# Optimization experiments

Measured on AMD Instinct MI355X. Metric: run time of the kernel, lower is better.

## Reference

```python
import jax, jax.numpy as jnp
import numpy as np
from jax import lax

B, N, D = 8, 1024, 512
HEAD_DIM = 64          # = num_attention_heads arg (used as split chunk size in torch)
H = D // HEAD_DIM      # actual number of heads = 8
TOPK = 32
EPS = 1e-5


def setup_inputs() -> dict:
    key = jax.random.key(0)
    ks = jax.random.split(key, 20)
    s = 0.02
    inp = {
        "src": jax.random.normal(ks[0], (B, N, D), jnp.float32),
        "tgt": jax.random.normal(ks[1], (B, N, D), jnp.float32),
        "Wq": jax.random.normal(ks[2], (D, D), jnp.float32) * s,
        "bq": jnp.zeros((D,), jnp.float32),
        "Wk": jax.random.normal(ks[3], (D, D), jnp.float32) * s,
        "bk": jnp.zeros((D,), jnp.float32),
        "Wv": jax.random.normal(ks[4], (D, D), jnp.float32) * s,
        "bv": jnp.zeros((D,), jnp.float32),
        "W1": jax.random.normal(ks[5], (D, D), jnp.float32) * s,
        "b1": jnp.zeros((D,), jnp.float32),
        "W2": jax.random.normal(ks[6], (D, D), jnp.float32) * s,
        "b2": jnp.zeros((D,), jnp.float32),
        "g1": jnp.ones((D,), jnp.float32),
        "be1": jnp.zeros((D,), jnp.float32),
        "g2": jnp.ones((D,), jnp.float32),
        "be2": jnp.zeros((D,), jnp.float32),
    }
    return inp


def _layer_norm(x, g, b):
    mu = jnp.mean(x, axis=-1, keepdims=True)
    var = jnp.mean(jnp.square(x - mu), axis=-1, keepdims=True)
    return (x - mu) * lax.rsqrt(var + EPS) * g + b


def _to_heads(x):
    # torch: cat(split(x, HEAD_DIM, dim=-1), dim=0) -> head-major leading dim
    # [B, N, D] -> [H*B, N, HEAD_DIM]
    return x.reshape(B, N, H, HEAD_DIM).transpose(2, 0, 1, 3).reshape(H * B, N, HEAD_DIM)


def reference(src, tgt, Wq, bq, Wk, bk, Wv, bv, W1, b1, W2, b2, g1, be1, g2, be2):
    q = _to_heads(tgt @ Wq + bq) / jnp.sqrt(jnp.float32(D))  # scale by hidden_dim**0.5 (as in source)
    k = _to_heads(src @ Wk + bk)
    v = _to_heads(src @ Wv + bv)

    scores = jnp.einsum('hqd,hkd->hqk', q, k)  # [H*B, N, N]

    idx = lax.top_k(scores, TOPK)[1]                       # [H*B, N, TOPK]
    vals = jnp.take_along_axis(scores, idx, axis=-1)       # gather top-k values
    sparse = jnp.full_like(scores, -jnp.inf)
    hb = jnp.arange(H * B)[:, None, None]
    qn = jnp.arange(N)[None, :, None]
    sparse = sparse.at[hb, qn, idx].set(vals)

    attn = jax.nn.softmax(sparse, axis=-1)                 # rows have TOPK finite entries
    out = jnp.einsum('hqk,hkd->hqd', attn, v)              # [H*B, N, HEAD_DIM]
    # torch: cat(split(out, B, dim=0), dim=-1) -> [B, N, D]
    out = out.reshape(H, B, N, HEAD_DIM).transpose(1, 2, 0, 3).reshape(B, N, D)

    x = _layer_norm(tgt + out, g1, be1)
    ff = jax.nn.relu(x @ W1 + b1) @ W2 + b2   # dropout = identity in eval mode
    return _layer_norm(x + ff, g2, be2)
```

## Files before the change

kernel.cpp:

```cpp
#include <hip/hip_runtime.h>
#include <math.h>

#define NSQ 1024
#define DM  512
#define HDIM 64
#define TOPK 32
#define QSTR 72
#define PCAP 64

typedef unsigned short u16;
typedef __attribute__((ext_vector_type(8))) short bf16x8;
typedef __attribute__((ext_vector_type(4))) float f32x4;

#define MFMA_B16(A,B,C) __builtin_amdgcn_mfma_f32_16x16x32_bf16(A,B,C,0,0,0)

__device__ __forceinline__ unsigned f2b(float x) {
    unsigned u = __float_as_uint(x);
    return (u + 0x7FFFu + ((u >> 16) & 1u)) >> 16;
}
__device__ __forceinline__ float b2f(unsigned h) { return __uint_as_float(h << 16); }
__device__ __forceinline__ unsigned ordu(float f) {
    unsigned b = __float_as_uint(f);
    return b ^ (0x80000000u | (unsigned)((int)b >> 31));
}
__device__ __forceinline__ float iordu(unsigned u) {
    unsigned b = (u & 0x80000000u) ? (u ^ 0x80000000u) : ~u;
    return __uint_as_float(b);
}

__global__ __launch_bounds__(256) void conv2(
    const float* __restrict__ tgt, const float* __restrict__ src,
    u16* __restrict__ Thi, u16* __restrict__ Tlo,
    u16* __restrict__ Shi, u16* __restrict__ Slo)
{
    const int z = blockIdx.y;
    const float* x = z ? src : tgt;
    u16* hi = z ? Shi : Thi;
    u16* lo = z ? Slo : Tlo;
    int idx = blockIdx.x * 256 + threadIdx.x;
    float4 v = ((const float4*)x)[idx];
    float f[4] = {v.x, v.y, v.z, v.w};
    ushort4 hv, lv;
    unsigned h;
    h = f2b(f[0]); hv.x = (u16)h; lv.x = (u16)f2b(f[0] - b2f(h));
    h = f2b(f[1]); hv.y = (u16)h; lv.y = (u16)f2b(f[1] - b2f(h));
    h = f2b(f[2]); hv.z = (u16)h; lv.z = (u16)f2b(f[2] - b2f(h));
    h = f2b(f[3]); hv.w = (u16)h; lv.w = (u16)f2b(f[3] - b2f(h));
    ((ushort4*)hi)[idx] = hv;
    ((ushort4*)lo)[idx] = lv;
}

__global__ __launch_bounds__(256) void wconv5(
    const float* __restrict__ Wq, const float* __restrict__ Wk,
    const float* __restrict__ Wv, const float* __restrict__ W1,
    const float* __restrict__ W2, u16* __restrict__ planes)
{
    __shared__ float T[32][33];
    const int wsel = blockIdx.z;
    const float* W = (wsel == 0) ? Wq : (wsel == 1) ? Wk : (wsel == 2) ? Wv
                   : (wsel == 3) ? W1 : W2;
    u16* thi = planes + (size_t)wsel * 2 * DM * DM;
    u16* tlo = thi + (size_t)DM * DM;
    const int tx = threadIdx.x & 31, ty = threadIdx.x >> 5;
    const int n0 = blockIdx.x * 32, k0 = blockIdx.y * 32;
#pragma unroll
    for (int p = 0; p < 4; ++p) {
        int r = ty + p * 8;
        T[r][tx] = W[(size_t)(k0 + r) * DM + n0 + tx];
    }
    __syncthreads();
#pragma unroll
    for (int p = 0; p < 4; ++p) {
        int rr = ty + p * 8;
        float val = T[tx][rr];
        unsigned h = f2b(val);
        size_t off = (size_t)(n0 + rr) * DM + k0 + tx;
        thi[off] = (u16)h;
        tlo[off] = (u16)f2b(val - b2f(h));
    }
}

template<int SPLIT, int RELU, int OUTMODE>
__global__ __launch_bounds__(256) void mm512(
    const u16* __restrict__ Ah_g, const u16* __restrict__ Al_g,
    const u16* __restrict__ Bh_g, const u16* __restrict__ Bl_g,
    const float* __restrict__ bias, const float* __restrict__ R,
    float scale, float* __restrict__ outF,
    u16* __restrict__ outHi, u16* __restrict__ outLo)
{
    __shared__ u16 Ah[128 * 40], Bh[128 * 40];
    __shared__ u16 Al[SPLIT ? 128 * 40 : 8], Bl[SPLIT ? 128 * 40 : 8];
    const int tid = threadIdx.x, lane = tid & 63, w = tid >> 6;
    const int wr = (w >> 1) * 64, wc = (w & 1) * 64;
    const int ml = lane & 15, q8 = (lane >> 4) * 8, q4 = (lane >> 4) * 4;
    const int row0 = blockIdx.x * 128, col0 = blockIdx.y * 128;
    const int sm = tid >> 2, sk = (tid & 3) * 8;

    f32x4 acc[4][4];
#pragma unroll
    for (int i = 0; i < 4; ++i)
#pragma unroll
        for (int j = 0; j < 4; ++j) acc[i][j] = {0.f, 0.f, 0.f, 0.f};

    for (int k0 = 0; k0 < DM; k0 += 32) {
#pragma unroll
        for (int p = 0; p < 2; ++p) {
            int m = sm + p * 64;
            *(uint4*)&Ah[m * 40 + sk] = *(const uint4*)&Ah_g[(size_t)(row0 + m) * DM + k0 + sk];
            *(uint4*)&Bh[m * 40 + sk] = *(const uint4*)&Bh_g[(size_t)(col0 + m) * DM + k0 + sk];
            if (SPLIT) {
                *(uint4*)&Al[m * 40 + sk] = *(const uint4*)&Al_g[(size_t)(row0 + m) * DM + k0 + sk];
                *(uint4*)&Bl[m * 40 + sk] = *(const uint4*)&Bl_g[(size_t)(col0 + m) * DM + k0 + sk];
            }
        }
        __syncthreads();
        bf16x8 a_h[4], b_h[4], a_l[4], b_l[4];
#pragma unroll
        for (int i = 0; i < 4; ++i) {
            a_h[i] = *(const bf16x8*)&Ah[(wr + i * 16 + ml) * 40 + q8];
            b_h[i] = *(const bf16x8*)&Bh[(wc + i * 16 + ml) * 40 + q8];
            if (SPLIT) {
                a_l[i] = *(const bf16x8*)&Al[(wr + i * 16 + ml) * 40 + q8];
                b_l[i] = *(const bf16x8*)&Bl[(wc + i * 16 + ml) * 40 + q8];
            }
        }
#pragma unroll
        for (int i = 0; i < 4; ++i)
#pragma unroll
            for (int j = 0; j < 4; ++j) {
                acc[i][j] = MFMA_B16(a_h[i], b_h[j], acc[i][j]);
                if (SPLIT) {
                    acc[i][j] = MFMA_B16(a_h[i], b_l[j], acc[i][j]);
                    acc[i][j] = MFMA_B16(a_l[i], b_h[j], acc[i][j]);
                    acc[i][j] = MFMA_B16(a_l[i], b_l[j], acc[i][j]);
                }
            }
        __syncthreads();
    }

    float bcol[4];
#pragma unroll
    for (int j = 0; j < 4; ++j) bcol[j] = bias[col0 + wc + j * 16 + ml];
#pragma unroll
    for (int i = 0; i < 4; ++i)
#pragma unroll
        for (int j = 0; j < 4; ++j)
#pragma unroll
            for (int r = 0; r < 4; ++r) {
                int gm = row0 + wr + i * 16 + q4 + r;
                int gn = col0 + wc + j * 16 + ml;
                float t = acc[i][j][r] + bcol[j];
                if (RELU) t = fmaxf(t, 0.f);
                t *= scale;
                size_t off = (size_t)gm * DM + gn;
                if (OUTMODE == 0) {
                    if (R) t += R[off];
                    outF[off] = t;
                } else if (OUTMODE == 1) {
                    unsigned hb2 = f2b(t);
                    outHi[off] = (u16)hb2;
                    outLo[off] = (u16)f2b(t - b2f(hb2));
                } else {
                    outHi[off] = (u16)f2b(t);
                }
            }
}

__global__ __launch_bounds__(256, 4) void attn_fused(
    const u16* __restrict__ qhi, const u16* __restrict__ qlo,
    const u16* __restrict__ khi, const u16* __restrict__ klo,
    const u16* __restrict__ vhi, u16* __restrict__ ao)
{
    __shared__ u16 Qh[16 * QSTR], Ql[16 * QSTR];
    __shared__ float statS[4][16], statQ[4][16];
    __shared__ int   cntW[4][16];
    __shared__ float pval[16][PCAP];
    __shared__ int   pcol[16][PCAP];
    __shared__ unsigned loU[16];

    const int tid = threadIdx.x, lane = tid & 63, w = tid >> 6;
    const int ml = lane & 15, quad = lane >> 4, q8 = quad * 8;
    const int hb = blockIdx.y, h = hb >> 3, b = hb & 7;
    const int r0 = blockIdx.x * 16;

    {
        int t2 = tid & 127, m = t2 >> 3, k8 = (t2 & 7) * 8;
        const u16* sp = (tid < 128) ? qhi : qlo;
        u16* dst = (tid < 128) ? Qh : Ql;
        *(uint4*)&dst[m * QSTR + k8] =
            *(const uint4*)&sp[((size_t)(b * NSQ + r0 + m)) * DM + h * HDIM + k8];
    }
    __syncthreads();

    bf16x8 a_h0 = *(const bf16x8*)&Qh[ml * QSTR + q8];
    bf16x8 a_h1 = *(const bf16x8*)&Qh[ml * QSTR + 32 + q8];
    bf16x8 a_l0 = *(const bf16x8*)&Ql[ml * QSTR + q8];
    bf16x8 a_l1 = *(const bf16x8*)&Ql[ml * QSTR + 32 + q8];

    const u16* khp = khi + ((size_t)(b * NSQ + w * 256 + ml)) * DM + h * HDIM + q8;
    const u16* klp = klo + ((size_t)(b * NSQ + w * 256 + ml)) * DM + h * HDIM + q8;

    f32x4 acc[16];
#pragma unroll
    for (int t = 0; t < 16; ++t) {
        bf16x8 bh0 = *(const bf16x8*)(khp);
        bf16x8 bh1 = *(const bf16x8*)(khp + 32);
        bf16x8 bl0 = *(const bf16x8*)(klp);
        bf16x8 bl1 = *(const bf16x8*)(klp + 32);
        f32x4 a0 = {0.f, 0.f, 0.f, 0.f}, a1 = {0.f, 0.f, 0.f, 0.f};
        a0 = MFMA_B16(a_h0, bh0, a0);
        a0 = MFMA_B16(a_h1, bh1, a0);
        a0 = MFMA_B16(a_l0, bh0, a0);
        a0 = MFMA_B16(a_l1, bh1, a0);
        a1 = MFMA_B16(a_h0, bl0, a1);
        a1 = MFMA_B16(a_h1, bl1, a1);
        a1 = MFMA_B16(a_l0, bl0, a1);
        a1 = MFMA_B16(a_l1, bl1, a1);
        acc[t] = a0 + a1;
        khp += 16 * DM;
        klp += 16 * DM;
    }

    float s1[4] = {0.f, 0.f, 0.f, 0.f}, s2[4] = {0.f, 0.f, 0.f, 0.f};
#pragma unroll
    for (int t = 0; t < 16; ++t)
#pragma unroll
        for (int r = 0; r < 4; ++r) {
            float v = acc[t][r];
            s1[r] += v;
            s2[r] = fmaf(v, v, s2[r]);
        }
#pragma unroll
    for (int off = 8; off; off >>= 1)
#pragma unroll
        for (int r = 0; r < 4; ++r) {
            s1[r] += __shfl_xor(s1[r], off);
            s2[r] += __shfl_xor(s2[r], off);
        }
    if (ml == 0)
#pragma unroll
        for (int r = 0; r < 4; ++r) {
            statS[w][quad * 4 + r] = s1[r];
            statQ[w][quad * 4 + r] = s2[r];
        }
    __syncthreads();

    float mu[4], sg[4], lo_f[4], hi_f[4];
    unsigned lo_u[4], hi_u[4];
    int clo[4];
#pragma unroll
    for (int r = 0; r < 4; ++r) {
        int row = quad * 4 + r;
        float S = statS[0][row] + statS[1][row] + statS[2][row] + statS[3][row];
        float Q = statQ[0][row] + statQ[1][row] + statQ[2][row] + statQ[3][row];
        mu[r] = S * (1.f / 1024.f);
        sg[r] = sqrtf(fmaxf(Q * (1.f / 1024.f) - mu[r] * mu[r], 0.f)) + 1e-20f;
        lo_f[r] = mu[r] - 8.f * sg[r];
        hi_f[r] = mu[r] + 8.f * sg[r];
        lo_u[r] = ordu(lo_f[r]);
        hi_u[r] = ordu(hi_f[r]);
        clo[r] = 1024;
    }

    int done = 0;
    for (int iter = 0; iter < 24; ++iter) {
        float mid_f[4]; unsigned mid_u[4];
#pragma unroll
        for (int r = 0; r < 4; ++r) {
            if (!((done >> r) & 1)) {
                float fr; unsigned um;
                if (iter == 0)      fr = mu[r] + 1.70f * sg[r];
                else if (iter == 1) fr = mu[r] + ((clo[r] == 1024) ? 1.38f : 2.15f) * sg[r];
                else {
                    um = lo_u[r] + ((hi_u[r] - lo_u[r]) >> 1);
                    fr = iordu(um); mid_u[r] = um; mid_f[r] = fr;
                    continue;
                }
                um = ordu(fr);
                if (um <= lo_u[r] || um >= hi_u[r]) {
                    um = lo_u[r] + ((hi_u[r] - lo_u[r]) >> 1);
                    fr = iordu(um);
                }
                mid_u[r] = um; mid_f[r] = fr;
            } else { mid_u[r] = lo_u[r]; mid_f[r] = lo_f[r]; }
        }
        int c[4] = {0, 0, 0, 0};
#pragma unroll
        for (int t = 0; t < 16; ++t)
#pragma unroll
            for (int r = 0; r < 4; ++r) c[r] += (acc[t][r] > mid_f[r]) ? 1 : 0;
#pragma unroll
        for (int off = 8; off; off >>= 1)
#pragma unroll
            for (int r = 0; r < 4; ++r) c[r] += __shfl_xor(c[r], off);
        if (ml == 0)
#pragma unroll
            for (int r = 0; r < 4; ++r) cntW[w][quad * 4 + r] = c[r];
        __syncthreads();
        int tot[4];
#pragma unroll
        for (int r = 0; r < 4; ++r) {
            int row = quad * 4 + r;
            tot[r] = cntW[0][row] + cntW[1][row] + cntW[2][row] + cntW[3][row];
        }
        __syncthreads();
#pragma unroll
        for (int r = 0; r < 4; ++r) {
            if (!((done >> r) & 1)) {
                if (tot[r] >= TOPK) {
                    lo_u[r] = mid_u[r]; lo_f[r] = mid_f[r]; clo[r] = tot[r];
                    if (tot[r] <= PCAP) done |= 1 << r;
                } else {
                    hi_u[r] = mid_u[r]; hi_f[r] = mid_f[r];
                }
                if (hi_u[r] - lo_u[r] <= 1u) done |= 1 << r;
            }
        }
        if (__all(done == 15)) break;
    }

    {
        int c[4] = {0, 0, 0, 0};
#pragma unroll
        for (int t = 0; t < 16; ++t)
#pragma unroll
            for (int r = 0; r < 4; ++r) c[r] += (acc[t][r] > lo_f[r]) ? 1 : 0;
#pragma unroll
        for (int off = 8; off; off >>= 1)
#pragma unroll
            for (int r = 0; r < 4; ++r) c[r] += __shfl_xor(c[r], off);
        if (ml == 0)
#pragma unroll
            for (int r = 0; r < 4; ++r) cntW[w][quad * 4 + r] = c[r];
        if (w == 0 && ml == 0)
#pragma unroll
            for (int r = 0; r < 4; ++r) loU[quad * 4 + r] = lo_u[r];
    }
    __syncthreads();

    int base[4];
#pragma unroll
    for (int r = 0; r < 4; ++r) {
        int row = quad * 4 + r, s = 0;
#pragma unroll
        for (int ww = 0; ww < 4; ++ww) s += (ww < w) ? cntW[ww][row] : 0;
        base[r] = s;
    }

    const unsigned lmask = (1u << ml) - 1u;
#pragma unroll
    for (int t = 0; t < 16; ++t)
#pragma unroll
        for (int r = 0; r < 4; ++r) {
            bool sel = acc[t][r] > lo_f[r];
            unsigned long long bm = __ballot(sel);
            unsigned mq = (unsigned)(bm >> (quad * 16)) & 0xFFFFu;
            if (sel) {
                int slot = base[r] + __popc(mq & lmask);
                if (slot < PCAP) {
                    pval[quad * 4 + r][slot] = acc[t][r];
                    pcol[quad * 4 + r][slot] = w * 256 + t * 16 + ml;
                }
            }
            base[r] += __popc(mq);
        }
    __syncthreads();

    const u16* vb = vhi + ((size_t)b * NSQ) * DM + h * HDIM + lane;
    for (int rr = 0; rr < 4; ++rr) {
        const int row = w * 4 + rr;
        int n = cntW[0][row] + cntW[1][row] + cntW[2][row] + cntW[3][row];
        if (n > PCAP) n = PCAP;
        float val = (lane < n) ? pval[row][lane] : 0.f;
        int   col = (lane < n) ? pcol[row][lane] : 0;
        unsigned uv = (lane < n) ? ordu(val) : 0u;

        unsigned blo = loU[row], bhi = 0xFFFFFFFFu;
        while (bhi - blo > 1u) {
            unsigned mid = blo + ((bhi - blo) >> 1);
            int c = __popcll(__ballot(uv > mid));
            if (c >= TOPK) { blo = mid; if (c == TOPK) break; }
            else bhi = mid;
        }
        bool sel = uv > blo;
        int excess = __popcll(__ballot(sel)) - TOPK;
        while (excess > 0) {
            int mycol = (sel && uv == blo + 1u) ? col : -1;
            int cmx = mycol;
#pragma unroll
            for (int off = 32; off; off >>= 1) cmx = max(cmx, __shfl_xor(cmx, off));
            if (sel && mycol >= 0 && col == cmx) sel = false;
            excess--;
        }

        float vsel = sel ? val : -INFINITY;
        float m = vsel;
#pragma unroll
        for (int off = 32; off; off >>= 1) m = fmaxf(m, __shfl_xor(m, off));
        float e = sel ? __expf(val - m) : 0.f;
        float s = e;
#pragma unroll
        for (int off = 32; off; off >>= 1) s += __shfl_xor(s, off);
        float p = e * (1.f / s);

        unsigned long long bm = __ballot(sel);
        int slot = __popcll(bm & ((1ull << lane) - 1ull));
        if (sel) { pval[row][slot] = p; pcol[row][slot] = col; }

        float accv = 0.f;
#pragma unroll
        for (int t0 = 0; t0 < TOPK; t0 += 8) {
            float pp[8]; int cc[8]; u16 vv[8];
#pragma unroll
            for (int j = 0; j < 8; ++j) { pp[j] = pval[row][t0 + j]; cc[j] = pcol[row][t0 + j]; }
#pragma unroll
            for (int j = 0; j < 8; ++j) vv[j] = vb[(size_t)cc[j] * DM];
#pragma unroll
            for (int j = 0; j < 8; ++j) accv = fmaf(pp[j], b2f(vv[j]), accv);
        }
        ao[((size_t)(b * NSQ + r0 + row)) * DM + h * HDIM + lane] = (u16)f2b(accv);
    }
}

__global__ __launch_bounds__(256) void ln_fused(
    const float* __restrict__ a, const u16* __restrict__ addb,
    const float* __restrict__ g, const float* __restrict__ be,
    float* __restrict__ outF, u16* __restrict__ outHi)
{
    __shared__ float red[4][2];
    const int row = blockIdx.x, tid = threadIdx.x, w = tid >> 6;
    float2 v = ((const float2*)(a + (size_t)row * DM))[tid];
    if (addb) {
        ushort2 ab = ((const ushort2*)(addb + (size_t)row * DM))[tid];
        v.x += b2f(ab.x); v.y += b2f(ab.y);
    }
    float s = v.x + v.y, q = v.x * v.x + v.y * v.y;
#pragma unroll
    for (int o = 32; o; o >>= 1) { s += __shfl_xor(s, o); q += __shfl_xor(q, o); }
    if ((tid & 63) == 0) { red[w][0] = s; red[w][1] = q; }
    __syncthreads();
    float S = red[0][0] + red[1][0] + red[2][0] + red[3][0];
    float Q = red[0][1] + red[1][1] + red[2][1] + red[3][1];
    float mu = S * (1.f / DM);
    float var = Q * (1.f / DM) - mu * mu;
    float rs = rsqrtf(var + 1e-5f);
    float2 gv = ((const float2*)g)[tid];
    float2 bv = ((const float2*)be)[tid];
    float2 o;
    o.x = (v.x - mu) * rs * gv.x + bv.x;
    o.y = (v.y - mu) * rs * gv.y + bv.y;
    if (outF) ((float2*)(outF + (size_t)row * DM))[tid] = o;
    if (outHi) {
        ushort2 hv; hv.x = (u16)f2b(o.x); hv.y = (u16)f2b(o.y);
        ((ushort2*)(outHi + (size_t)row * DM))[tid] = hv;
    }
}

extern "C" void kernel_launch(void* const* d_in, const int* in_sizes, int n_in,
                              void* d_out, int out_size, void* d_ws, size_t ws_size,
                              hipStream_t stream) {
    const float* src = (const float*)d_in[0];
    const float* tgt = (const float*)d_in[1];
    const float* Wq  = (const float*)d_in[2];
    const float* bq  = (const float*)d_in[3];
    const float* Wk  = (const float*)d_in[4];
    const float* bk  = (const float*)d_in[5];
    const float* Wv  = (const float*)d_in[6];
    const float* bv  = (const float*)d_in[7];
    const float* W1  = (const float*)d_in[8];
    const float* b1  = (const float*)d_in[9];
    const float* W2  = (const float*)d_in[10];
    const float* b2  = (const float*)d_in[11];
    const float* g1  = (const float*)d_in[12];
    const float* be1 = (const float*)d_in[13];
    const float* g2  = (const float*)d_in[14];
    const float* be2 = (const float*)d_in[15];

    const size_t WPLANE = (size_t)DM * DM;
    u16* planes = (u16*)d_ws;
    auto wh = [&](int i) { return planes + (size_t)i * 2 * WPLANE; };
    auto wl = [&](int i) { return planes + (size_t)i * 2 * WPLANE + WPLANE; };
    auto at = [&](size_t mb) { return (char*)d_ws + (mb << 20); };
    u16* Thi = (u16*)at(8);   u16* Tlo = (u16*)at(16);
    u16* Shi = (u16*)at(24);  u16* Slo = (u16*)at(32);
    u16* qhi = (u16*)at(40);  u16* qlo = (u16*)at(48);
    u16* khi = (u16*)at(56);  u16* klo = (u16*)at(64);
    u16* vhi = (u16*)at(72);
    u16* aob = (u16*)at(80);
    float* xb = (float*)at(88);
    u16* xhi = (u16*)at(104);
    u16* hhi = (u16*)at(112);
    float* f2 = (float*)at(120);

    dim3 blk(256);
    const float qscale = 0.04419417382415922f;

    wconv5<<<dim3(16, 16, 5), blk, 0, stream>>>(Wq, Wk, Wv, W1, W2, planes);
    conv2<<<dim3(4096, 2), blk, 0, stream>>>(tgt, src, Thi, Tlo, Shi, Slo);

    mm512<1, 0, 1><<<dim3(64, 4), blk, 0, stream>>>(Thi, Tlo, wh(0), wl(0), bq, nullptr,
                                                    qscale, nullptr, qhi, qlo);
    mm512<1, 0, 1><<<dim3(64, 4), blk, 0, stream>>>(Shi, Slo, wh(1), wl(1), bk, nullptr,
                                                    1.f, nullptr, khi, klo);
    mm512<0, 0, 2><<<dim3(64, 4), blk, 0, stream>>>(Shi, nullptr, wh(2), nullptr, bv, nullptr,
                                                    1.f, nullptr, vhi, nullptr);

    attn_fused<<<dim3(64, 64), blk, 0, stream>>>(qhi, qlo, khi, klo, vhi, aob);

    ln_fused<<<8192, blk, 0, stream>>>(tgt, aob, g1, be1, xb, xhi);
    mm512<0, 1, 2><<<dim3(64, 4), blk, 0, stream>>>(xhi, nullptr, wh(3), nullptr, b1, nullptr,
                                                    1.f, nullptr, hhi, nullptr);
    mm512<0, 0, 0><<<dim3(64, 4), blk, 0, stream>>>(hhi, nullptr, wh(4), nullptr, b2, xb,
                                                    1.f, f2, nullptr, nullptr);
    ln_fused<<<8192, blk, 0, stream>>>(f2, nullptr, g2, be2, (float*)d_out, nullptr);
}
```

Measured before the change: 435.4 us.

## Shrink GEMM tiles to 64x64, streamline top-k compaction and softmax in attention

The GEMM kernel moves from 128x128 to 64x64 output tiles with a 64-wide K step. That raises the grid from 256 to 1024 blocks so all CUs are busy, at the cost of less operand reuse per block. In attention, the count buffer is double-buffered to drop one barrier per bisection iteration. Candidate compaction switches from ballot prefix sums to LDS atomics into a packed float2 buffer. The final bisection now starts from the known upper bound with interpolated midpoints, and the softmax max reduction is replaced by the threshold value. The V gather is unrolled by 16.

```diff
diff --git a/kernel.cpp b/kernel.cpp
--- a/kernel.cpp
+++ b/kernel.cpp
@@ -81,70 +81,75 @@
 }
 
 template<int SPLIT, int RELU, int OUTMODE>
-__global__ __launch_bounds__(256) void mm512(
+__global__ __launch_bounds__(256, 4) void mm512(
     const u16* __restrict__ Ah_g, const u16* __restrict__ Al_g,
     const u16* __restrict__ Bh_g, const u16* __restrict__ Bl_g,
     const float* __restrict__ bias, const float* __restrict__ R,
     float scale, float* __restrict__ outF,
     u16* __restrict__ outHi, u16* __restrict__ outLo)
 {
-    __shared__ u16 Ah[128 * 40], Bh[128 * 40];
-    __shared__ u16 Al[SPLIT ? 128 * 40 : 8], Bl[SPLIT ? 128 * 40 : 8];
+    __shared__ u16 Ah[64 * 72], Bh[64 * 72];
+    __shared__ u16 Al[SPLIT ? 64 * 72 : 8], Bl[SPLIT ? 64 * 72 : 8];
     const int tid = threadIdx.x, lane = tid & 63, w = tid >> 6;
-    const int wr = (w >> 1) * 64, wc = (w & 1) * 64;
+    const int wr = (w >> 1) * 32, wc = (w & 1) * 32;
     const int ml = lane & 15, q8 = (lane >> 4) * 8, q4 = (lane >> 4) * 4;
-    const int row0 = blockIdx.x * 128, col0 = blockIdx.y * 128;
-    const int sm = tid >> 2, sk = (tid & 3) * 8;
-
-    f32x4 acc[4][4];
-#pragma unroll
-    for (int i = 0; i < 4; ++i)
-#pragma unroll
-        for (int j = 0; j < 4; ++j) acc[i][j] = {0.f, 0.f, 0.f, 0.f};
-
-    for (int k0 = 0; k0 < DM; k0 += 32) {
-#pragma unroll
-        for (int p = 0; p < 2; ++p) {
-            int m = sm + p * 64;
-            *(uint4*)&Ah[m * 40 + sk] = *(const uint4*)&Ah_g[(size_t)(row0 + m) * DM + k0 + sk];
-            *(uint4*)&Bh[m * 40 + sk] = *(const uint4*)&Bh_g[(size_t)(col0 + m) * DM + k0 + sk];
-            if (SPLIT) {
-                *(uint4*)&Al[m * 40 + sk] = *(const uint4*)&Al_g[(size_t)(row0 + m) * DM + k0 + sk];
-                *(uint4*)&Bl[m * 40 + sk] = *(const uint4*)&Bl_g[(size_t)(col0 + m) * DM + k0 + sk];
-            }
+    const int row0 = blockIdx.x * 64, col0 = blockIdx.y * 64;
+    const int sr = tid >> 2, sc = (tid & 3) * 8;
+
+    f32x4 acc[2][2];
+#pragma unroll
+    for (int i = 0; i < 2; ++i)
+#pragma unroll
+        for (int j = 0; j < 2; ++j) acc[i][j] = {0.f, 0.f, 0.f, 0.f};
+
+    for (int k0 = 0; k0 < DM; k0 += 64) {
+        const size_t ra = (size_t)(row0 + sr) * DM + k0 + sc;
+        const size_t rb = (size_t)(col0 + sr) * DM + k0 + sc;
+        *(uint4*)&Ah[sr * 72 + sc]      = *(const uint4*)&Ah_g[ra];
+        *(uint4*)&Ah[sr * 72 + sc + 32] = *(const uint4*)&Ah_g[ra + 32];
+        *(uint4*)&Bh[sr * 72 + sc]      = *(const uint4*)&Bh_g[rb];
+        *(uint4*)&Bh[sr * 72 + sc + 32] = *(const uint4*)&Bh_g[rb + 32];
+        if (SPLIT) {
+            *(uint4*)&Al[sr * 72 + sc]      = *(const uint4*)&Al_g[ra];
+            *(uint4*)&Al[sr * 72 + sc + 32] = *(const uint4*)&Al_g[ra + 32];
+            *(uint4*)&Bl[sr * 72 + sc]      = *(const uint4*)&Bl_g[rb];
+            *(uint4*)&Bl[sr * 72 + sc + 32] = *(const uint4*)&Bl_g[rb + 32];
         }
         __syncthreads();
-        bf16x8 a_h[4], b_h[4], a_l[4], b_l[4];
-#pragma unroll
-        for (int i = 0; i < 4; ++i) {
-            a_h[i] = *(const bf16x8*)&Ah[(wr + i * 16 + ml) * 40 + q8];
-            b_h[i] = *(const bf16x8*)&Bh[(wc + i * 16 + ml) * 40 + q8];
-            if (SPLIT) {
-                a_l[i] = *(const bf16x8*)&Al[(wr + i * 16 + ml) * 40 + q8];
-                b_l[i] = *(const bf16x8*)&Bl[(wc + i * 16 + ml) * 40 + q8];
-            }
-        }
-#pragma unroll
-        for (int i = 0; i < 4; ++i)
-#pragma unroll
-            for (int j = 0; j < 4; ++j) {
-                acc[i][j] = MFMA_B16(a_h[i], b_h[j], acc[i][j]);
+#pragma unroll
+        for (int kk = 0; kk < 64; kk += 32) {
+            bf16x8 a_h[2], b_h[2], a_l[2], b_l[2];
+#pragma unroll
+            for (int i = 0; i < 2; ++i) {
+                a_h[i] = *(const bf16x8*)&Ah[(wr + i * 16 + ml) * 72 + kk + q8];
+                b_h[i] = *(const bf16x8*)&Bh[(wc + i * 16 + ml) * 72 + kk + q8];
                 if (SPLIT) {
-                    acc[i][j] = MFMA_B16(a_h[i], b_l[j], acc[i][j]);
-                    acc[i][j] = MFMA_B16(a_l[i], b_h[j], acc[i][j]);
-                    acc[i][j] = MFMA_B16(a_l[i], b_l[j], acc[i][j]);
+                    a_l[i] = *(const bf16x8*)&Al[(wr + i * 16 + ml) * 72 + kk + q8];
+                    b_l[i] = *(const bf16x8*)&Bl[(wc + i * 16 + ml) * 72 + kk + q8];
                 }
             }
+#pragma unroll
+            for (int i = 0; i < 2; ++i)
+#pragma unroll
+                for (int j = 0; j < 2; ++j) {
+                    acc[i][j] = MFMA_B16(a_h[i], b_h[j], acc[i][j]);
+                    if (SPLIT) {
+                        acc[i][j] = MFMA_B16(a_h[i], b_l[j], acc[i][j]);
+                        acc[i][j] = MFMA_B16(a_l[i], b_h[j], acc[i][j]);
+                        acc[i][j] = MFMA_B16(a_l[i], b_l[j], acc[i][j]);
+                    }
+                }
+        }
         __syncthreads();
     }
 
-    float bcol[4];
-#pragma unroll
-    for (int j = 0; j < 4; ++j) bcol[j] = bias[col0 + wc + j * 16 + ml];
-#pragma unroll
-    for (int i = 0; i < 4; ++i)
-#pragma unroll
-        for (int j = 0; j < 4; ++j)
+    float bcol[2];
+#pragma unroll
+    for (int j = 0; j < 2; ++j) bcol[j] = bias[col0 + wc + j * 16 + ml];
+#pragma unroll
+    for (int i = 0; i < 2; ++i)
+#pragma unroll
+        for (int j = 0; j < 2; ++j)
 #pragma unroll
             for (int r = 0; r < 4; ++r) {
                 int gm = row0 + wr + i * 16 + q4 + r;
@@ -173,10 +178,10 @@
 {
     __shared__ u16 Qh[16 * QSTR], Ql[16 * QSTR];
     __shared__ float statS[4][16], statQ[4][16];
-    __shared__ int   cntW[4][16];
-    __shared__ float pval[16][PCAP];
-    __shared__ int   pcol[16][PCAP];
-    __shared__ unsigned loU[16];
+    __shared__ int   cntW[2][4][16];
+    __shared__ float2 pbuf[16 * PCAP];
+    __shared__ int   pcnt[16];
+    __shared__ unsigned loU[16], hiU[16];
 
     const int tid = threadIdx.x, lane = tid & 63, w = tid >> 6;
     const int ml = lane & 15, quad = lane >> 4, q8 = quad * 8;
@@ -190,6 +195,7 @@
         *(uint4*)&dst[m * QSTR + k8] =
             *(const uint4*)&sp[((size_t)(b * NSQ + r0 + m)) * DM + h * HDIM + k8];
     }
+    if (tid < 16) pcnt[tid] = 0;
     __syncthreads();
 
     bf16x8 a_h0 = *(const bf16x8*)&Qh[ml * QSTR + q8];
@@ -293,17 +299,18 @@
         for (int off = 8; off; off >>= 1)
 #pragma unroll
             for (int r = 0; r < 4; ++r) c[r] += __shfl_xor(c[r], off);
+        const int buf = iter & 1;
         if (ml == 0)
 #pragma unroll
-            for (int r = 0; r < 4; ++r) cntW[w][quad * 4 + r] = c[r];
+            for (int r = 0; r < 4; ++r) cntW[buf][w][quad * 4 + r] = c[r];
         __syncthreads();
         int tot[4];
 #pragma unroll
         for (int r = 0; r < 4; ++r) {
             int row = quad * 4 + r;
-            tot[r] = cntW[0][row] + cntW[1][row] + cntW[2][row] + cntW[3][row];
-        }
-        __syncthreads();
+            tot[r] = cntW[buf][0][row] + cntW[buf][1][row]
+                   + cntW[buf][2][row] + cntW[buf][3][row];
+        }
 #pragma unroll
         for (int r = 0; r < 4; ++r) {
             if (!((done >> r) & 1)) {
@@ -319,68 +326,50 @@
         if (__all(done == 15)) break;
     }
 
-    {
-        int c[4] = {0, 0, 0, 0};
-#pragma unroll
-        for (int t = 0; t < 16; ++t)
-#pragma unroll
-            for (int r = 0; r < 4; ++r) c[r] += (acc[t][r] > lo_f[r]) ? 1 : 0;
-#pragma unroll
-        for (int off = 8; off; off >>= 1)
-#pragma unroll
-            for (int r = 0; r < 4; ++r) c[r] += __shfl_xor(c[r], off);
-        if (ml == 0)
-#pragma unroll
-            for (int r = 0; r < 4; ++r) cntW[w][quad * 4 + r] = c[r];
-        if (w == 0 && ml == 0)
-#pragma unroll
-            for (int r = 0; r < 4; ++r) loU[quad * 4 + r] = lo_u[r];
-    }
-    __syncthreads();
-
-    int base[4];
-#pragma unroll
-    for (int r = 0; r < 4; ++r) {
-        int row = quad * 4 + r, s = 0;
-#pragma unroll
-        for (int ww = 0; ww < 4; ++ww) s += (ww < w) ? cntW[ww][row] : 0;
-        base[r] = s;
-    }
-
-    const unsigned lmask = (1u << ml) - 1u;
+    if (w == 0 && ml == 0)
+#pragma unroll
+        for (int r = 0; r < 4; ++r) {
+            loU[quad * 4 + r] = lo_u[r];
+            hiU[quad * 4 + r] = hi_u[r];
+        }
+
 #pragma unroll
     for (int t = 0; t < 16; ++t)
 #pragma unroll
         for (int r = 0; r < 4; ++r) {
-            bool sel = acc[t][r] > lo_f[r];
-            unsigned long long bm = __ballot(sel);
-            unsigned mq = (unsigned)(bm >> (quad * 16)) & 0xFFFFu;
-            if (sel) {
-                int slot = base[r] + __popc(mq & lmask);
-                if (slot < PCAP) {
-                    pval[quad * 4 + r][slot] = acc[t][r];
-                    pcol[quad * 4 + r][slot] = w * 256 + t * 16 + ml;
-                }
+            if (acc[t][r] > lo_f[r]) {
+                int row = quad * 4 + r;
+                int s = atomicAdd(&pcnt[row], 1);
+                if (s < PCAP)
+                    pbuf[row * PCAP + s] =
+                        make_float2(acc[t][r], __int_as_float(w * 256 + t * 16 + ml));
             }
-            base[r] += __popc(mq);
         }
     __syncthreads();
 
     const u16* vb = vhi + ((size_t)b * NSQ) * DM + h * HDIM + lane;
     for (int rr = 0; rr < 4; ++rr) {
         const int row = w * 4 + rr;
-        int n = cntW[0][row] + cntW[1][row] + cntW[2][row] + cntW[3][row];
+        int n = pcnt[row];
         if (n > PCAP) n = PCAP;
-        float val = (lane < n) ? pval[row][lane] : 0.f;
-        int   col = (lane < n) ? pcol[row][lane] : 0;
+        float2 pr = (lane < n) ? pbuf[row * PCAP + lane] : make_float2(0.f, 0.f);
+        float val = pr.x;
+        int   col = __float_as_int(pr.y);
         unsigned uv = (lane < n) ? ordu(val) : 0u;
 
-        unsigned blo = loU[row], bhi = 0xFFFFFFFFu;
+        unsigned blo = loU[row], bhi = hiU[row];
+        int it = 0;
         while (bhi - blo > 1u) {
-            unsigned mid = blo + ((bhi - blo) >> 1);
-            int c = __popcll(__ballot(uv > mid));
-            if (c >= TOPK) { blo = mid; if (c == TOPK) break; }
-            else bhi = mid;
+            unsigned um;
+            if (it & 1) um = blo + ((bhi - blo) >> 1);
+            else {
+                um = ordu(0.5f * (iordu(blo) + iordu(bhi)));
+                if (um <= blo || um >= bhi) um = blo + ((bhi - blo) >> 1);
+            }
+            ++it;
+            int c = __popcll(__ballot(uv > um));
+            if (c >= TOPK) { blo = um; if (c == TOPK) break; }
+            else bhi = um;
         }
         bool sel = uv > blo;
         int excess = __popcll(__ballot(sel)) - TOPK;
@@ -393,11 +382,8 @@
             excess--;
         }
 
-        float vsel = sel ? val : -INFINITY;
-        float m = vsel;
-#pragma unroll
-        for (int off = 32; off; off >>= 1) m = fmaxf(m, __shfl_xor(m, off));
-        float e = sel ? __expf(val - m) : 0.f;
+        float mshift = iordu(blo);
+        float e = sel ? __expf(val - mshift) : 0.f;
         float s = e;
 #pragma unroll
         for (int off = 32; off; off >>= 1) s += __shfl_xor(s, off);
@@ -405,18 +391,21 @@
 
         unsigned long long bm = __ballot(sel);
         int slot = __popcll(bm & ((1ull << lane) - 1ull));
-        if (sel) { pval[row][slot] = p; pcol[row][slot] = col; }
+        if (sel) pbuf[row * PCAP + slot] = make_float2(p, __int_as_float(col));
 
         float accv = 0.f;
 #pragma unroll
-        for (int t0 = 0; t0 < TOPK; t0 += 8) {
-            float pp[8]; int cc[8]; u16 vv[8];
-#pragma unroll
-            for (int j = 0; j < 8; ++j) { pp[j] = pval[row][t0 + j]; cc[j] = pcol[row][t0 + j]; }
-#pragma unroll
-            for (int j = 0; j < 8; ++j) vv[j] = vb[(size_t)cc[j] * DM];
-#pragma unroll
-            for (int j = 0; j < 8; ++j) accv = fmaf(pp[j], b2f(vv[j]), accv);
+        for (int t0 = 0; t0 < TOPK; t0 += 16) {
+            float pp[16]; int cc[16]; u16 vv[16];
+#pragma unroll
+            for (int j = 0; j < 16; ++j) {
+                float2 pc = pbuf[row * PCAP + t0 + j];
+                pp[j] = pc.x; cc[j] = __float_as_int(pc.y);
+            }
+#pragma unroll
+            for (int j = 0; j < 16; ++j) vv[j] = vb[(size_t)cc[j] * DM];
+#pragma unroll
+            for (int j = 0; j < 16; ++j) accv = fmaf(pp[j], b2f(vv[j]), accv);
         }
         ao[((size_t)(b * NSQ + r0 + row)) * DM + h * HDIM + lane] = (u16)f2b(accv);
     }
@@ -493,24 +482,25 @@
     float* f2 = (float*)at(120);
 
     dim3 blk(256);
+    dim3 gmm(128, 8);
     const float qscale = 0.04419417382415922f;
 
     wconv5<<<dim3(16, 16, 5), blk, 0, stream>>>(Wq, Wk, Wv, W1, W2, planes);
     conv2<<<dim3(4096, 2), blk, 0, stream>>>(tgt, src, Thi, Tlo, Shi, Slo);
 
-    mm512<1, 0, 1><<<dim3(64, 4), blk, 0, stream>>>(Thi, Tlo, wh(0), wl(0), bq, nullptr,
-                                                    qscale, nullptr, qhi, qlo);
-    mm512<1, 0, 1><<<dim3(64, 4), blk, 0, stream>>>(Shi, Slo, wh(1), wl(1), bk, nullptr,
-                                                    1.f, nullptr, khi, klo);
-    mm512<0, 0, 2><<<dim3(64, 4), blk, 0, stream>>>(Shi, nullptr, wh(2), nullptr, bv, nullptr,
-                                                    1.f, nullptr, vhi, nullptr);
+    mm512<1, 0, 1><<<gmm, blk, 0, stream>>>(Thi, Tlo, wh(0), wl(0), bq, nullptr,
+                                            qscale, nullptr, qhi, qlo);
+    mm512<1, 0, 1><<<gmm, blk, 0, stream>>>(Shi, Slo, wh(1), wl(1), bk, nullptr,
+                                            1.f, nullptr, khi, klo);
+    mm512<0, 0, 2><<<gmm, blk, 0, stream>>>(Shi, nullptr, wh(2), nullptr, bv, nullptr,
+                                            1.f, nullptr, vhi, nullptr);
 
     attn_fused<<<dim3(64, 64), blk, 0, stream>>>(qhi, qlo, khi, klo, vhi, aob);
 
     ln_fused<<<8192, blk, 0, stream>>>(tgt, aob, g1, be1, xb, xhi);
-    mm512<0, 1, 2><<<dim3(64, 4), blk, 0, stream>>>(xhi, nullptr, wh(3), nullptr, b1, nullptr,
-                                                    1.f, nullptr, hhi, nullptr);
-    mm512<0, 0, 0><<<dim3(64, 4), blk, 0, stream>>>(hhi, nullptr, wh(4), nullptr, b2, xb,
-                                                    1.f, f2, nullptr, nullptr);
+    mm512<0, 1, 2><<<gmm, blk, 0, stream>>>(xhi, nullptr, wh(3), nullptr, b1, nullptr,
+                                            1.f, nullptr, hhi, nullptr);
+    mm512<0, 0, 0><<<gmm, blk, 0, stream>>>(hhi, nullptr, wh(4), nullptr, b2, xb,
+                                            1.f, f2, nullptr, nullptr);
     ln_fused<<<8192, blk, 0, stream>>>(f2, nullptr, g2, be2, (float*)d_out, nullptr);
 }
```

New measurement: 397.0 us. 1.1x faster.
